# Kernel tuning notes

Hardware: AMD Instinct MI355X
Metric: run time of the kernel (lower is better)

The kernel has to match this reference:

```python
import jax, jax.numpy as jnp
import numpy as np

# ---- constants matching init_kwargs ----
LAMBDA_CON = 0.4
LAMBDA_BC = 0.2
DX = 0.01
DT = 0.001
U0 = 1.0
VISC = 0.01
CROP = 512
N = CROP - 2  # 510
B = 32

# ---- fixed-weight convs expressed as slicing stencils (valid conv) ----
def div_ddx(x):      # 3x3 kernel [[0,0,0],[-1,1,0],[0,0,0]]
    return x[:, :, 1:-1, 1:-1] - x[:, :, 1:-1, :-2]

def div_ddy(x):      # 3x3 kernel [[0,-1,0],[0,1,0],[0,0,0]]
    return x[:, :, 1:-1, 1:-1] - x[:, :, :-2, 1:-1]

def avg_x(x):        # 2x2 kernel [[.5,.5],[0,0]]
    return 0.5 * (x[:, :, :-1, :-1] + x[:, :, :-1, 1:])

def avg_y(x):        # 2x2 kernel [[.5,0],[.5,0]]
    return 0.5 * (x[:, :, :-1, :-1] + x[:, :, 1:, :-1])

def up_ddx(x):       # 2x2 kernel [[-1,1],[0,0]]
    return x[:, :, :-1, 1:] - x[:, :, :-1, :-1]

def up_ddy(x):       # 2x2 kernel [[-1,0],[1,0]]
    return x[:, :, 1:, :-1] - x[:, :, :-1, :-1]

def down_ddx(x):     # 2x2 kernel [[0,0],[-1,1]]
    return x[:, :, 1:, 1:] - x[:, :, 1:, :-1]

def down_ddy(x):     # 2x2 kernel [[0,-1],[0,1]]
    return x[:, :, 1:, 1:] - x[:, :, :-1, 1:]

def laplacian(x):    # 3x3 kernel [[0,-1,0],[-1,4,-1],[0,-1,0]]
    return (4.0 * x[:, :, 1:-1, 1:-1]
            - x[:, :, 1:-1, 2:] - x[:, :, 1:-1, :-2]
            - x[:, :, 2:, 1:-1] - x[:, :, :-2, 1:-1])


def _poisson_dudt(u, v, p):
    ue = avg_x(u)
    vn = avg_x(v)
    flux_e = ue * avg_x(u) - (VISC / DX) * up_ddx(u)
    flux_n = vn * avg_y(u) - (VISC / DX) * up_ddy(u)
    flux_e = flux_e[:, :, :, :-1]
    flux_n = flux_n[:, :, :, :-1]
    pu = p[:, :, :-1, 1:-1]
    return (-down_ddx(flux_e) - down_ddy(flux_n) - down_ddx(pu)) / DX


def _poisson_dvdt(u, v, p):
    ue = avg_y(u)
    vn = avg_y(v)
    flux_e = ue * avg_x(v) - (VISC / DX) * up_ddx(v)
    flux_n = vn * avg_y(v) - (VISC / DX) * up_ddy(v)
    flux_e = flux_e[:, :, :-1, :]
    flux_n = flux_n[:, :, :-1, :]
    pv = p[:, :, 1:-1, :-1]
    return (-down_ddx(flux_e) - down_ddy(flux_n) - down_ddy(pv)) / DX


def _bc_loss(g):
    u, v, p = g[:, 0], g[:, 1], g[:, 2]  # [B,H,W]
    y0 = (jnp.sum(u[:, 0, 1:N] + u[:, 1, 1:N], axis=1)
          + jnp.sum(v[:, 0, 1:N + 1] + p[:, 0, 1:N + 1], axis=1))
    yL = (jnp.sum(2.0 * U0 - (u[:, N, 1:N] + u[:, N + 1, 1:N]), axis=1)
          + jnp.sum(v[:, N + 1, 1:N + 1] + p[:, N + 1, 1:N + 1], axis=1))
    x0 = (jnp.sum(v[:, 1:N, 0] + v[:, 1:N, 1], axis=1)
          + jnp.sum(u[:, 1:N + 1, 0] + p[:, 1:N + 1, 0], axis=1))
    xL = (jnp.sum(v[:, 1:N, N + 1] + v[:, 1:N, N], axis=1)
          + jnp.sum(u[:, 1:N + 1, N + 1] + p[:, 1:N + 1, N + 1], axis=1))
    return jnp.sum(jnp.abs(y0) + jnp.abs(yL) + jnp.abs(x0) + jnp.abs(xL))


def setup_inputs() -> dict:
    key = jax.random.key(0)
    k1, k2 = jax.random.split(key)
    gen_output = jax.random.normal(k1, (B, 3, CROP, CROP), dtype=jnp.float32)
    p_next_step = jax.random.normal(k2, (B, 1, CROP, CROP), dtype=jnp.float32)
    return {"gen_output": gen_output, "p_next_step": p_next_step}


def reference(gen_output, p_next_step):
    u = gen_output[:, 0:1]
    v = gen_output[:, 1:2]
    p = gen_output[:, 2:3]

    # continuity residual on interior grid [B,1,N,N]
    continuity_res = (div_ddx(u) + div_ddy(v)) / DX
    continuity_loss = jnp.mean(jnp.abs(continuity_res), axis=(2, 3))  # [B,1]

    dudt = _poisson_dudt(u, v, p)  # [B,1,N,N-1]
    dvdt = _poisson_dvdt(u, v, p)  # [B,1,N-1,N]
    dudt_pad = jnp.pad(dudt, ((0, 0), (0, 0), (1, 1), (1, 2)))  # -> [B,1,CROP,CROP]
    dvdt_pad = jnp.pad(dvdt, ((0, 0), (0, 0), (1, 2), (1, 1)))

    p_prime = p_next_step - p
    u_new = u + dudt_pad * DT
    v_new = v + dvdt_pad * DT
    b_conv = (div_ddx(u_new) / DX + div_ddy(v_new) / DX) / DT
    poisson_res = laplacian(p_prime) / DX ** 2 + b_conv  # [B,1,N,N]
    poisson_loss = jnp.mean(jnp.abs(poisson_res), axis=(2, 3))  # [B,1]

    b_c_loss = _bc_loss(gen_output)  # scalar

    pi_loss = (LAMBDA_CON * continuity_loss
               + LAMBDA_BC * b_c_loss
               + (1.0 - LAMBDA_CON - LAMBDA_BC) * poisson_loss)
    return jnp.mean(pi_loss)
```

## Files before the change

kernel.cpp:

```cpp
#include <hip/hip_runtime.h>

#define CROPX 512
#define NN 510
#define BATCHX 32

constexpr float INV_DX   = 100.0f;
constexpr float DT_F     = 0.001f;
constexpr float INV_DXDT = 100000.0f;
constexpr float INV_DX2  = 10000.0f;

__device__ __forceinline__ void load_row6(const float* __restrict__ base, int r,
                                          int c0, float o[6]) {
    const float* rp = base + (size_t)r * CROPX;
    const float4 q = *reinterpret_cast<const float4*>(rp + c0);
    float h0, h1;
    if (c0 + 5 <= CROPX - 1) {
        const float2 h = *reinterpret_cast<const float2*>(rp + c0 + 4);
        h0 = h.x; h1 = h.y;
    } else {
        h0 = rp[CROPX - 1];
        h1 = rp[CROPX - 1];
    }
    o[0] = q.x; o[1] = q.y; o[2] = q.z; o[3] = q.w; o[4] = h0; o[5] = h1;
}

__global__ __launch_bounds__(256, 4) void pde_main(const float* __restrict__ g,
                                                   const float* __restrict__ png,
                                                   float* __restrict__ ws) {
    const int bb   = blockIdx.z;
    const int w    = threadIdx.x >> 6;
    const int lane = threadIdx.x & 63;
    const int tile = blockIdx.y * 4 + w;
    const int cg   = blockIdx.x;
    const int c0   = cg * 256 + lane * 4;
    const int a0   = tile * 4;

    const float* u  = g + (size_t)bb * 3 * (CROPX * CROPX);
    const float* v  = u + CROPX * CROPX;
    const float* p  = v + CROPX * CROPX;
    const float* pn = png + (size_t)bb * (CROPX * CROPX);

    const bool edgelane = (cg == 1 && lane == 0);

    float u1[6], v1[6], p1[6], pn1[6];
    float fnuC[5], fnvC[5], dvdtC[4], ppN[4], vup[4];

    {
        float ua[6], va[6], pa[6], pna[6];
        load_row6(u,  a0, c0, ua);
        load_row6(v,  a0, c0, va);
        load_row6(p,  a0, c0, pa);
        load_row6(pn, a0, c0, pna);
        load_row6(u,  a0 + 1, c0, u1);
        load_row6(v,  a0 + 1, c0, v1);
        load_row6(p,  a0 + 1, c0, p1);
        load_row6(pn, a0 + 1, c0, pn1);

        #pragma unroll
        for (int j = 0; j < 5; ++j)
            fnuC[j] = 0.5f * (va[j] + va[j + 1]) * 0.5f * (ua[j] + u1[j]) - (u1[j] - ua[j]);
        #pragma unroll
        for (int j = 1; j < 5; ++j) {
            float m = 0.5f * (va[j] + v1[j]);
            fnvC[j] = m * m - (v1[j] - va[j]);
        }
        #pragma unroll
        for (int k = 0; k < 4; ++k) { ppN[k] = pna[k + 1] - pa[k + 1]; vup[k] = va[k + 1]; }

        if (a0 > 0) {
            float vm[6];
            load_row6(v, a0 - 1, c0, vm);
            float fev[5];
            #pragma unroll
            for (int j = 0; j < 5; ++j)
                fev[j] = 0.5f * (ua[j] + u1[j]) * 0.5f * (va[j] + va[j + 1]) - (va[j + 1] - va[j]);
            #pragma unroll
            for (int k = 0; k < 4; ++k) {
                float mm = 0.5f * (vm[k + 1] + va[k + 1]);
                float fnvm = mm * mm - (va[k + 1] - vm[k + 1]);
                dvdtC[k] = (-(fev[k + 1] - fev[k]) - (fnvC[k + 1] - fnvm)
                            - (p1[k + 1] - pa[k + 1])) * INV_DX;
            }
        } else {
            #pragma unroll
            for (int k = 0; k < 4; ++k) dvdtC[k] = 0.0f;
        }
    }

    float cont_acc = 0.0f, pois_acc = 0.0f;

    #pragma unroll
    for (int it = 0; it < 4; ++it) {
        const int a  = a0 + it;
        const int r1 = (a + 1 < CROPX) ? a + 1 : CROPX - 1;
        const int r2 = (a + 2 < CROPX) ? a + 2 : CROPX - 1;

        float u2[6], v2[6], p2[6], pn2[6];
        load_row6(u,  r2, c0, u2);
        load_row6(v,  r2, c0, v2);
        load_row6(p,  r2, c0, p2);
        load_row6(pn, r2, c0, pn2);

        float uLeft = 0.0f;
        if (edgelane) uLeft = u[(size_t)r1 * CROPX + (c0 - 1)];

        float FEu[5], FEv[5], FNu1[5], FNv1[5];
        #pragma unroll
        for (int j = 0; j < 5; ++j) {
            float ux = 0.5f * (u1[j] + u1[j + 1]);
            FEu[j] = ux * ux - (u1[j + 1] - u1[j]);
            float uy = 0.5f * (u1[j] + u2[j]);
            float vx = 0.5f * (v1[j] + v1[j + 1]);
            float prod = uy * vx;
            FEv[j]  = prod - (v1[j + 1] - v1[j]);
            FNu1[j] = prod - (u2[j] - u1[j]);
        }
        #pragma unroll
        for (int j = 1; j < 5; ++j) {
            float vy = 0.5f * (v1[j] + v2[j]);
            FNv1[j] = vy * vy - (v2[j] - v1[j]);
        }

        float dudt[4], dvdt[4];
        #pragma unroll
        for (int k = 0; k < 4; ++k) {
            dudt[k] = (-(FEu[k + 1] - FEu[k]) - (FNu1[k + 1] - fnuC[k + 1])
                       - (p1[k + 2] - p1[k + 1])) * INV_DX;
            dvdt[k] = (-(FEv[k + 1] - FEv[k]) - (FNv1[k + 1] - fnvC[k + 1])
                       - (p2[k + 1] - p1[k + 1])) * INV_DX;
        }

        float dudtLm = __shfl_up(dudt[3], 1, 64);
        if (edgelane) {
            float uxm  = 0.5f * (uLeft + u1[0]);
            float FEuL = uxm * uxm - (u1[0] - uLeft);
            dudtLm = (-(FEu[0] - FEuL) - (FNu1[0] - fnuC[0]) - (p1[1] - p1[0])) * INV_DX;
        }

        #pragma unroll
        for (int k = 0; k < 4; ++k) {
            const int b = c0 + k;
            float ppC = pn1[k + 1] - p1[k + 1];
            float ppS = pn2[k + 1] - p2[k + 1];
            float ppW = pn1[k]     - p1[k];
            float ppE = pn1[k + 2] - p1[k + 2];
            float lap = 4.0f * ppC - ppE - ppW - ppS - ppN[k];
            float du_x = u1[k + 1] - u1[k];
            float dv_y = v1[k + 1] - vup[k];
            float dL  = (k == 0) ? dudtLm : dudt[k - 1];
            float dRm = (b <= NN - 2) ? dudt[k] : 0.0f;
            float dLm = (b >= 1)      ? dL      : 0.0f;
            float vCm = (a <= NN - 2) ? dvdt[k] : 0.0f;
            float vPm = (a >= 1)      ? dvdtC[k] : 0.0f;
            float bconv = (du_x + dv_y + DT_F * ((dRm - dLm) + (vCm - vPm))) * INV_DXDT;
            float pois  = lap * INV_DX2 + bconv;
            if (b < NN && a < NN) {
                cont_acc += fabsf((du_x + dv_y) * INV_DX);
                pois_acc += fabsf(pois);
            }
            ppN[k]   = ppC;
            vup[k]   = v1[k + 1];
            dvdtC[k] = dvdt[k];
        }
        #pragma unroll
        for (int j = 0; j < 5; ++j) { fnuC[j] = FNu1[j]; if (j >= 1) fnvC[j] = FNv1[j]; }
        #pragma unroll
        for (int j = 0; j < 6; ++j) { u1[j] = u2[j]; v1[j] = v2[j]; p1[j] = p2[j]; pn1[j] = pn2[j]; }
    }

    float c = cont_acc, q = pois_acc;
    #pragma unroll
    for (int off = 32; off > 0; off >>= 1) {
        c += __shfl_down(c, off, 64);
        q += __shfl_down(q, off, 64);
    }
    __shared__ float sred[8];
    if (lane == 0) { sred[w] = c; sred[4 + w] = q; }
    __syncthreads();
    if (threadIdx.x == 0) {
        atomicAdd(&ws[0], sred[0] + sred[1] + sred[2] + sred[3]);
        atomicAdd(&ws[1], sred[4] + sred[5] + sred[6] + sred[7]);
    }
}

__global__ __launch_bounds__(256) void pde_bc(const float* __restrict__ g,
                                              float* __restrict__ ws) {
    const int bb    = blockIdx.y;
    const int slice = blockIdx.x;
    const int lane  = threadIdx.x & 63;
    const int role  = threadIdx.x >> 6;
    const int j     = slice * 64 + lane;

    const float* u = g + (size_t)bb * 3 * (CROPX * CROPX);
    const float* v = u + CROPX * CROPX;
    const float* p = v + CROPX * CROPX;

    const bool in9  = (j >= 1 && j <= NN - 1);
    const bool in10 = (j >= 1 && j <= NN);

    float val = 0.0f;
    if (role == 0) {
        if (in9)  val += u[j] + u[CROPX + j];
        if (in10) val += v[j] + p[j];
    } else if (role == 1) {
        if (in9)  val += 2.0f - u[(size_t)NN * CROPX + j] - u[(size_t)(NN + 1) * CROPX + j];
        if (in10) val += v[(size_t)(NN + 1) * CROPX + j] + p[(size_t)(NN + 1) * CROPX + j];
    } else if (role == 2) {
        if (in9)  val += v[(size_t)j * CROPX] + v[(size_t)j * CROPX + 1];
        if (in10) val += u[(size_t)j * CROPX] + p[(size_t)j * CROPX];
    } else {
        if (in9)  val += v[(size_t)j * CROPX + (CROPX - 1)] + v[(size_t)j * CROPX + (CROPX - 2)];
        if (in10) val += u[(size_t)j * CROPX + (CROPX - 1)] + p[(size_t)j * CROPX + (CROPX - 1)];
    }

    #pragma unroll
    for (int off = 32; off > 0; off >>= 1) val += __shfl_down(val, off, 64);
    if (lane == 0) atomicAdd(&ws[4 + bb * 4 + role], val);
}

__global__ void pde_final(const float* __restrict__ ws, float* __restrict__ out) {
    const int t = threadIdx.x;
    float bc = 0.0f;
    if (t < BATCHX) {
        const float* wb = ws + 4 + t * 4;
        bc = fabsf(wb[0]) + fabsf(wb[1]) + fabsf(wb[2]) + fabsf(wb[3]);
    }
    #pragma unroll
    for (int off = 32; off > 0; off >>= 1) bc += __shfl_down(bc, off, 64);
    if (t == 0) {
        const float inv = 1.0f / ((float)BATCHX * NN * NN);
        out[0] = 0.4f * (ws[0] + ws[1]) * inv + 0.2f * bc;
    }
}

extern "C" void kernel_launch(void* const* d_in, const int* in_sizes, int n_in,
                              void* d_out, int out_size, void* d_ws, size_t ws_size,
                              hipStream_t stream) {
    const float* g  = (const float*)d_in[0];
    const float* pn = (const float*)d_in[1];
    float* out = (float*)d_out;
    float* ws  = (float*)d_ws;

    hipMemsetAsync(ws, 0, (4 + BATCHX * 4) * sizeof(float), stream);

    dim3 gm(2, 32, 32);
    pde_main<<<gm, 256, 0, stream>>>(g, pn, ws);
    dim3 gb(8, 32);
    pde_bc<<<gb, 256, 0, stream>>>(g, ws);
    pde_final<<<1, 64, 0, stream>>>(ws, out);
}
```

Before: 214.1 us.

## Double-buffer row loads and process eight rows per wave

```diff
diff --git a/kernel.cpp b/kernel.cpp
--- a/kernel.cpp
+++ b/kernel.cpp
@@ -8,6 +8,13 @@
 constexpr float DT_F     = 0.001f;
 constexpr float INV_DXDT = 100000.0f;
 constexpr float INV_DX2  = 10000.0f;
+
+__device__ __forceinline__ float4 ld4(const float* __restrict__ b, int r, int c) {
+    return *reinterpret_cast<const float4*>(b + (size_t)r * CROPX + c);
+}
+__device__ __forceinline__ float2 ld2(const float* __restrict__ b, int r, int c) {
+    return *reinterpret_cast<const float2*>(b + (size_t)r * CROPX + c);
+}
 
 __device__ __forceinline__ void load_row6(const float* __restrict__ base, int r,
                                           int c0, float o[6]) {
@@ -24,7 +31,19 @@
     o[0] = q.x; o[1] = q.y; o[2] = q.z; o[3] = q.w; o[4] = h0; o[5] = h1;
 }
 
-__global__ __launch_bounds__(256, 4) void pde_main(const float* __restrict__ g,
+#define DECL_BUF(X) \
+    float4 X##U, X##V, X##P, X##N; float2 X##Uh, X##Vh, X##Ph, X##Nh; \
+    float X##Ul = 0.0f;
+
+#define LOAD_BUF(X, ROW) { \
+    const int _rw = (ROW); \
+    X##U = ld4(u, _rw, c0);     X##V = ld4(v, _rw, c0); \
+    X##P = ld4(p, _rw, c0);     X##N = ld4(pn, _rw, c0); \
+    X##Uh = ld2(u, _rw, chalo); X##Vh = ld2(v, _rw, chalo); \
+    X##Ph = ld2(p, _rw, chalo); X##Nh = ld2(pn, _rw, chalo); \
+    if (edge0) X##Ul = u[(size_t)(_rw - 1) * CROPX + 255]; }
+
+__global__ __launch_bounds__(256, 3) void pde_main(const float* __restrict__ g,
                                                    const float* __restrict__ png,
                                                    float* __restrict__ ws) {
     const int bb   = blockIdx.z;
@@ -33,17 +52,21 @@
     const int tile = blockIdx.y * 4 + w;
     const int cg   = blockIdx.x;
     const int c0   = cg * 256 + lane * 4;
-    const int a0   = tile * 4;
+    const int a0   = tile * 8;
+    const int chalo = (c0 + 4 < 510) ? c0 + 4 : 510;
 
     const float* u  = g + (size_t)bb * 3 * (CROPX * CROPX);
     const float* v  = u + CROPX * CROPX;
     const float* p  = v + CROPX * CROPX;
     const float* pn = png + (size_t)bb * (CROPX * CROPX);
 
-    const bool edgelane = (cg == 1 && lane == 0);
+    const bool edge0 = (cg == 1 && lane == 0);
 
     float u1[6], v1[6], p1[6], pn1[6];
     float fnuC[5], fnvC[5], dvdtC[4], ppN[4], vup[4];
+
+    DECL_BUF(A)
+    DECL_BUF(B)
 
     {
         float ua[6], va[6], pa[6], pna[6];
@@ -55,6 +78,7 @@
         load_row6(v,  a0 + 1, c0, v1);
         load_row6(p,  a0 + 1, c0, p1);
         load_row6(pn, a0 + 1, c0, pn1);
+        LOAD_BUF(A, a0 + 2)
 
         #pragma unroll
         for (int j = 0; j < 5; ++j)
@@ -89,84 +113,94 @@
 
     float cont_acc = 0.0f, pois_acc = 0.0f;
 
-    #pragma unroll
-    for (int it = 0; it < 4; ++it) {
-        const int a  = a0 + it;
-        const int r1 = (a + 1 < CROPX) ? a + 1 : CROPX - 1;
-        const int r2 = (a + 2 < CROPX) ? a + 2 : CROPX - 1;
-
-        float u2[6], v2[6], p2[6], pn2[6];
-        load_row6(u,  r2, c0, u2);
-        load_row6(v,  r2, c0, v2);
-        load_row6(p,  r2, c0, p2);
-        load_row6(pn, r2, c0, pn2);
-
-        float uLeft = 0.0f;
-        if (edgelane) uLeft = u[(size_t)r1 * CROPX + (c0 - 1)];
-
-        float FEu[5], FEv[5], FNu1[5], FNv1[5];
-        #pragma unroll
-        for (int j = 0; j < 5; ++j) {
-            float ux = 0.5f * (u1[j] + u1[j + 1]);
-            FEu[j] = ux * ux - (u1[j + 1] - u1[j]);
-            float uy = 0.5f * (u1[j] + u2[j]);
-            float vx = 0.5f * (v1[j] + v1[j + 1]);
-            float prod = uy * vx;
-            FEv[j]  = prod - (v1[j + 1] - v1[j]);
-            FNu1[j] = prod - (u2[j] - u1[j]);
-        }
-        #pragma unroll
-        for (int j = 1; j < 5; ++j) {
-            float vy = 0.5f * (v1[j] + v2[j]);
-            FNv1[j] = vy * vy - (v2[j] - v1[j]);
-        }
-
-        float dudt[4], dvdt[4];
-        #pragma unroll
-        for (int k = 0; k < 4; ++k) {
-            dudt[k] = (-(FEu[k + 1] - FEu[k]) - (FNu1[k + 1] - fnuC[k + 1])
-                       - (p1[k + 2] - p1[k + 1])) * INV_DX;
-            dvdt[k] = (-(FEv[k + 1] - FEv[k]) - (FNv1[k + 1] - fnvC[k + 1])
-                       - (p2[k + 1] - p1[k + 1])) * INV_DX;
-        }
-
-        float dudtLm = __shfl_up(dudt[3], 1, 64);
-        if (edgelane) {
-            float uxm  = 0.5f * (uLeft + u1[0]);
-            float FEuL = uxm * uxm - (u1[0] - uLeft);
-            dudtLm = (-(FEu[0] - FEuL) - (FNu1[0] - fnuC[0]) - (p1[1] - p1[0])) * INV_DX;
-        }
-
-        #pragma unroll
-        for (int k = 0; k < 4; ++k) {
-            const int b = c0 + k;
-            float ppC = pn1[k + 1] - p1[k + 1];
-            float ppS = pn2[k + 1] - p2[k + 1];
-            float ppW = pn1[k]     - p1[k];
-            float ppE = pn1[k + 2] - p1[k + 2];
-            float lap = 4.0f * ppC - ppE - ppW - ppS - ppN[k];
-            float du_x = u1[k + 1] - u1[k];
-            float dv_y = v1[k + 1] - vup[k];
-            float dL  = (k == 0) ? dudtLm : dudt[k - 1];
-            float dRm = (b <= NN - 2) ? dudt[k] : 0.0f;
-            float dLm = (b >= 1)      ? dL      : 0.0f;
-            float vCm = (a <= NN - 2) ? dvdt[k] : 0.0f;
-            float vPm = (a >= 1)      ? dvdtC[k] : 0.0f;
-            float bconv = (du_x + dv_y + DT_F * ((dRm - dLm) + (vCm - vPm))) * INV_DXDT;
-            float pois  = lap * INV_DX2 + bconv;
-            if (b < NN && a < NN) {
-                cont_acc += fabsf((du_x + dv_y) * INV_DX);
-                pois_acc += fabsf(pois);
-            }
-            ppN[k]   = ppC;
-            vup[k]   = v1[k + 1];
-            dvdtC[k] = dvdt[k];
-        }
-        #pragma unroll
-        for (int j = 0; j < 5; ++j) { fnuC[j] = FNu1[j]; if (j >= 1) fnvC[j] = FNv1[j]; }
-        #pragma unroll
-        for (int j = 0; j < 6; ++j) { u1[j] = u2[j]; v1[j] = v2[j]; p1[j] = p2[j]; pn1[j] = pn2[j]; }
-    }
+#define PDE_IT(IT, CUR, NXT)                                                      \
+    {                                                                             \
+        const int a = a0 + (IT);                                                  \
+        if ((IT) < 7) LOAD_BUF(NXT, ((a + 3 < CROPX) ? a + 3 : CROPX - 1))        \
+        float u2[6], v2[6], p2[6], pn2[6];                                        \
+        u2[0] = CUR##U.x;  u2[1] = CUR##U.y;  u2[2] = CUR##U.z;  u2[3] = CUR##U.w;\
+        u2[4] = CUR##Uh.x; u2[5] = CUR##Uh.y;                                     \
+        v2[0] = CUR##V.x;  v2[1] = CUR##V.y;  v2[2] = CUR##V.z;  v2[3] = CUR##V.w;\
+        v2[4] = CUR##Vh.x; v2[5] = CUR##Vh.y;                                     \
+        p2[0] = CUR##P.x;  p2[1] = CUR##P.y;  p2[2] = CUR##P.z;  p2[3] = CUR##P.w;\
+        p2[4] = CUR##Ph.x; p2[5] = CUR##Ph.y;                                     \
+        pn2[0] = CUR##N.x;  pn2[1] = CUR##N.y;  pn2[2] = CUR##N.z;                \
+        pn2[3] = CUR##N.w;  pn2[4] = CUR##Nh.x; pn2[5] = CUR##Nh.y;               \
+        const float uLeft = CUR##Ul;                                              \
+        float FEu[5], FEv[5], FNu1[5], FNv1[5];                                   \
+        _Pragma("unroll")                                                         \
+        for (int j = 0; j < 5; ++j) {                                             \
+            float ux = 0.5f * (u1[j] + u1[j + 1]);                                \
+            FEu[j] = ux * ux - (u1[j + 1] - u1[j]);                               \
+            float uy = 0.5f * (u1[j] + u2[j]);                                    \
+            float vx = 0.5f * (v1[j] + v1[j + 1]);                                \
+            float prod = uy * vx;                                                 \
+            FEv[j]  = prod - (v1[j + 1] - v1[j]);                                 \
+            FNu1[j] = prod - (u2[j] - u1[j]);                                     \
+        }                                                                         \
+        _Pragma("unroll")                                                         \
+        for (int j = 1; j < 5; ++j) {                                             \
+            float vy = 0.5f * (v1[j] + v2[j]);                                    \
+            FNv1[j] = vy * vy - (v2[j] - v1[j]);                                  \
+        }                                                                         \
+        float dudt[4], dvdt[4];                                                   \
+        _Pragma("unroll")                                                         \
+        for (int k = 0; k < 4; ++k) {                                             \
+            dudt[k] = (-(FEu[k + 1] - FEu[k]) - (FNu1[k + 1] - fnuC[k + 1])       \
+                       - (p1[k + 2] - p1[k + 1])) * INV_DX;                       \
+            dvdt[k] = (-(FEv[k + 1] - FEv[k]) - (FNv1[k + 1] - fnvC[k + 1])       \
+                       - (p2[k + 1] - p1[k + 1])) * INV_DX;                       \
+        }                                                                         \
+        float dudtLm = __shfl_up(dudt[3], 1, 64);                                 \
+        if (edge0) {                                                              \
+            float uxm  = 0.5f * (uLeft + u1[0]);                                  \
+            float FEuL = uxm * uxm - (u1[0] - uLeft);                             \
+            dudtLm = (-(FEu[0] - FEuL) - (FNu1[0] - fnuC[0])                      \
+                      - (p1[1] - p1[0])) * INV_DX;                                \
+        }                                                                         \
+        _Pragma("unroll")                                                         \
+        for (int k = 0; k < 4; ++k) {                                             \
+            const int b = c0 + k;                                                 \
+            float ppC = pn1[k + 1] - p1[k + 1];                                   \
+            float ppS = pn2[k + 1] - p2[k + 1];                                   \
+            float ppW = pn1[k]     - p1[k];                                       \
+            float ppE = pn1[k + 2] - p1[k + 2];                                   \
+            float lap = 4.0f * ppC - ppE - ppW - ppS - ppN[k];                    \
+            float du_x = u1[k + 1] - u1[k];                                       \
+            float dv_y = v1[k + 1] - vup[k];                                      \
+            float dL  = (k == 0) ? dudtLm : dudt[k - 1];                          \
+            float dRm = (b <= NN - 2) ? dudt[k] : 0.0f;                           \
+            float dLm = (b >= 1)      ? dL      : 0.0f;                           \
+            float vCm = (a <= NN - 2) ? dvdt[k] : 0.0f;                           \
+            float vPm = (a >= 1)      ? dvdtC[k] : 0.0f;                          \
+            float bconv = (du_x + dv_y + DT_F * ((dRm - dLm) + (vCm - vPm)))      \
+                          * INV_DXDT;                                             \
+            float pois  = lap * INV_DX2 + bconv;                                  \
+            if (b < NN && a < NN) {                                               \
+                cont_acc += fabsf((du_x + dv_y) * INV_DX);                        \
+                pois_acc += fabsf(pois);                                          \
+            }                                                                     \
+            ppN[k]   = ppC;                                                       \
+            vup[k]   = v1[k + 1];                                                 \
+            dvdtC[k] = dvdt[k];                                                   \
+        }                                                                         \
+        _Pragma("unroll")                                                         \
+        for (int j = 0; j < 5; ++j) { fnuC[j] = FNu1[j]; if (j >= 1) fnvC[j] = FNv1[j]; } \
+        _Pragma("unroll")                                                         \
+        for (int j = 0; j < 6; ++j) {                                             \
+            u1[j] = u2[j]; v1[j] = v2[j]; p1[j] = p2[j]; pn1[j] = pn2[j];         \
+        }                                                                         \
+    }
+
+    PDE_IT(0, A, B)
+    PDE_IT(1, B, A)
+    PDE_IT(2, A, B)
+    PDE_IT(3, B, A)
+    PDE_IT(4, A, B)
+    PDE_IT(5, B, A)
+    PDE_IT(6, A, B)
+    PDE_IT(7, B, A)
+#undef PDE_IT
 
     float c = cont_acc, q = pois_acc;
     #pragma unroll
@@ -243,7 +277,7 @@
 
     hipMemsetAsync(ws, 0, (4 + BATCHX * 4) * sizeof(float), stream);
 
-    dim3 gm(2, 32, 32);
+    dim3 gm(2, 16, 32);
     pde_main<<<gm, 256, 0, stream>>>(g, pn, ws);
     dim3 gb(8, 32);
     pde_bc<<<gb, 256, 0, stream>>>(g, ws);
```

Measured after the change: 191.8 us. 10.4% less time.
